# Kernel optimization log

Hardware: AMD Instinct MI355X
Metric: run time of the kernel (lower is better)

The kernel has to match this reference:

```python
import jax, jax.numpy as jnp
import numpy as np
import math

N_COARSE, N_FINE = 8192, 32768
DEC_DIM, ENC_DIM, OUT_DIM, K = 256, 128, 128, 16
LN_EPS = 1e-5


def setup_inputs() -> dict:
    key = jax.random.key(0)
    ks = jax.random.split(key, 16)
    s = lambda fan_in: 1.0 / math.sqrt(fan_in)
    return {
        "decoder_features": jax.random.normal(ks[0], (N_COARSE, DEC_DIM), jnp.float32),
        "decoder_pos": jax.random.normal(ks[1], (N_COARSE, 3), jnp.float32),
        "encoder_features": jax.random.normal(ks[2], (N_FINE, ENC_DIM), jnp.float32),
        "encoder_pos": jax.random.normal(ks[3], (N_FINE, 3), jnp.float32),
        "encoder_labels": jax.random.randint(ks[4], (N_FINE,), 0, 13, jnp.int64),
        # params (torch nn.Linear default init scale)
        "Wq": jax.random.uniform(ks[5], (DEC_DIM, ENC_DIM), jnp.float32, -s(ENC_DIM), s(ENC_DIM)),
        "bq": jnp.zeros((DEC_DIM,), jnp.float32),
        "Wk": jax.random.uniform(ks[6], (DEC_DIM, DEC_DIM), jnp.float32, -s(DEC_DIM), s(DEC_DIM)),
        "bk": jnp.zeros((DEC_DIM,), jnp.float32),
        "Wv": jax.random.uniform(ks[7], (DEC_DIM, DEC_DIM), jnp.float32, -s(DEC_DIM), s(DEC_DIM)),
        "bv": jnp.zeros((DEC_DIM,), jnp.float32),
        "W1": jax.random.uniform(ks[8], (OUT_DIM, DEC_DIM + ENC_DIM), jnp.float32, -s(DEC_DIM + ENC_DIM), s(DEC_DIM + ENC_DIM)),
        "b1": jnp.zeros((OUT_DIM,), jnp.float32),
        "W2": jax.random.uniform(ks[9], (OUT_DIM, OUT_DIM), jnp.float32, -s(OUT_DIM), s(OUT_DIM)),
        "b2": jnp.zeros((OUT_DIM,), jnp.float32),
        "ln_g": jnp.ones((OUT_DIM,), jnp.float32),
        "ln_b": jnp.zeros((OUT_DIM,), jnp.float32),
    }


def _knn_indices(encoder_pos, decoder_pos, k):
    # For each fine (encoder) point, k nearest coarse (decoder) points.
    # squared distances [N_fine, N_coarse]
    d2 = (
        jnp.sum(encoder_pos * encoder_pos, axis=1, keepdims=True)
        - 2.0 * encoder_pos @ decoder_pos.T
        + jnp.sum(decoder_pos * decoder_pos, axis=1)[None, :]
    )
    _, idx = jax.lax.top_k(-d2, k)  # [N_fine, K]
    return idx


def reference(decoder_features, decoder_pos, encoder_features, encoder_pos,
              encoder_labels, Wq, bq, Wk, bk, Wv, bv, W1, b1, W2, b2, ln_g, ln_b):
    idx = _knn_indices(encoder_pos, decoder_pos, K)            # [Nf, K]
    nbr = decoder_features[idx]                                 # [Nf, K, Dd]
    query = encoder_features @ Wq.T + bq                        # [Nf, Dd]
    keys = nbr @ Wk.T + bk                                      # [Nf, K, Dd]
    values = nbr @ Wv.T + bv                                    # [Nf, K, Dd]
    scores = jnp.einsum('nd,nkd->nk', query, keys) / math.sqrt(DEC_DIM)
    # segment softmax over edges grouped by fine target == softmax over K
    weights = jax.nn.softmax(scores, axis=-1)                   # [Nf, K]
    agg = jnp.einsum('nk,nkd->nd', weights, values)             # [Nf, Dd]
    combined = jnp.concatenate([agg, encoder_features], axis=-1)
    h = jax.nn.relu(combined @ W1.T + b1)
    up = h @ W2.T + b2                                          # [Nf, out]
    mu = jnp.mean(up, axis=-1, keepdims=True)
    var = jnp.var(up, axis=-1, keepdims=True)
    out = (up - mu) * jax.lax.rsqrt(var + LN_EPS) * ln_g + ln_b
    # dropout is identity in eval mode
    return (out, encoder_pos, encoder_labels)
```

## Files before the change

kernel.cpp:

```cpp
#include <hip/hip_runtime.h>
#include <hip/hip_bf16.h>

typedef __hip_bfloat16 bf16;
typedef unsigned short u16;

#define NC 8192
#define NF 32768
#define KNN 16
#define FMAXV 3.402823466e+38f

__device__ __forceinline__ float bfbits2f(u16 u){
  union { unsigned u; float f; } x; x.u = ((unsigned)u) << 16; return x.f;
}

__global__ __launch_bounds__(256) void k_prep(const float* __restrict__ dpos,
                                              const float* __restrict__ W1,
                                              const float* __restrict__ W2,
                                              float4* __restrict__ pos4,
                                              float4* __restrict__ W1eSa,
                                              float4* __restrict__ W1eSb,
                                              float4* __restrict__ W2Sa,
                                              float4* __restrict__ W2Sb){
  int g = blockIdx.x * 256 + threadIdx.x;
  if (g < 8192){
    float x = dpos[g * 3 + 0], y = dpos[g * 3 + 1], z = dpos[g * 3 + 2];
    float dd = __fadd_rn(__fadd_rn(__fmul_rn(x,x), __fmul_rn(y,y)), __fmul_rn(z,z));
    pos4[g] = make_float4(x, y, z, dd * 0.5f);
  } else if (g < 10240){
    int f = g - 8192; int c4 = f >> 6, jg = f & 63;
    W1eSa[f] = ((const float4*)(W1 + (size_t)(2 * jg) * 384 + 256))[c4];
  } else if (g < 12288){
    int f = g - 10240; int c4 = f >> 6, jg = f & 63;
    W1eSb[f] = ((const float4*)(W1 + (size_t)(2 * jg + 1) * 384 + 256))[c4];
  } else if (g < 14336){
    int f = g - 12288; int c4 = f >> 6, jg = f & 63;
    W2Sa[f] = ((const float4*)(W2 + (size_t)(2 * jg) * 128))[c4];
  } else if (g < 16384){
    int f = g - 14336; int c4 = f >> 6, jg = f & 63;
    W2Sb[f] = ((const float4*)(W2 + (size_t)(2 * jg + 1) * 128))[c4];
  }
}

__global__ __launch_bounds__(256) void k_wprod(const float* __restrict__ Wk,
                                               const float* __restrict__ Wv,
                                               const float* __restrict__ Wq,
                                               const float* __restrict__ W1,
                                               const float* __restrict__ bk,
                                               const float* __restrict__ bv,
                                               const float* __restrict__ bq,
                                               float* __restrict__ WkqS,
                                               float* __restrict__ WvuS,
                                               float* __restrict__ bkq,
                                               float* __restrict__ bvu,
                                               float* __restrict__ wbq,
                                               float* __restrict__ sbq){
  __shared__ float red[256];
  int b = blockIdx.x, t = threadIdx.x;
  if (b < 128){
    int c = b;
    float acc = 0.f;
    for (int j = 0; j < 256; ++j)
      acc = fmaf(Wk[(size_t)j * 256 + t], Wq[(size_t)j * 128 + c], acc);
    WkqS[(size_t)((t >> 2) * 128 + c) * 4 + (t & 3)] = acc;
    red[t] = bk[t] * Wq[(size_t)t * 128 + c];
    __syncthreads();
    for (int s = 128; s > 0; s >>= 1){ if (t < s) red[t] += red[t + s]; __syncthreads(); }
    if (t == 0) bkq[c] = red[0];
  } else if (b < 256){
    int h = b - 128;
    float acc = 0.f;
    for (int c2 = 0; c2 < 256; ++c2)
      acc = fmaf(Wv[(size_t)c2 * 256 + t], W1[(size_t)h * 384 + c2], acc);
    WvuS[(size_t)((t >> 2) * 128 + h) * 4 + (t & 3)] = acc;
    red[t] = bv[t] * W1[(size_t)h * 384 + t];
    __syncthreads();
    for (int s = 128; s > 0; s >>= 1){ if (t < s) red[t] += red[t + s]; __syncthreads(); }
    if (t == 0) bvu[h] = red[0];
  } else {
    float acc = 0.f;
    for (int j = 0; j < 256; ++j)
      acc = fmaf(Wk[(size_t)j * 256 + t], bq[j], acc);
    wbq[t] = acc;
    red[t] = bk[t] * bq[t];
    __syncthreads();
    for (int s = 128; s > 0; s >>= 1){ if (t < s) red[t] += red[t + s]; __syncthreads(); }
    if (t == 0) sbq[0] = red[0];
  }
}

__global__ __launch_bounds__(256) void k_dec(const float* __restrict__ df,
                                             const float4* __restrict__ WkqS,
                                             const float4* __restrict__ WvuS,
                                             const float* __restrict__ bkq,
                                             const float* __restrict__ bvu,
                                             const float* __restrict__ wbq,
                                             const float* __restrict__ sbq,
                                             bf16* __restrict__ Zd, bf16* __restrict__ Ud,
                                             float* __restrict__ bqK){
  __shared__ float part[16][16];
  int t = threadIdx.x;
  int g0 = blockIdx.x * 16;
  int half = __builtin_amdgcn_readfirstlane(t >> 7);
  int c = t & 127;
  const float4* W = half ? WvuS : WkqS;
  float acc[16];
  #pragma unroll
  for (int p = 0; p < 16; ++p) acc[p] = 0.f;
  for (int j4 = 0; j4 < 64; ++j4){
    float4 w = W[j4 * 128 + c];
    #pragma unroll
    for (int p = 0; p < 16; ++p){
      float4 a = ((const float4*)(df + (size_t)(g0 + p) * 256))[j4];
      acc[p] += w.x*a.x + w.y*a.y + w.z*a.z + w.w*a.w;
    }
  }
  float bias = half ? bvu[c] : bkq[c];
  bf16* dst = half ? Ud : Zd;
  #pragma unroll
  for (int p = 0; p < 16; ++p)
    dst[(size_t)(g0 + p) * 128 + c] = __float2bfloat16(acc[p] + bias);
  {
    int r = t >> 4, seg = t & 15;
    float s = 0.f;
    const float* dr = df + (size_t)(g0 + r) * 256 + seg * 16;
    const float* wq = wbq + seg * 16;
    #pragma unroll
    for (int e = 0; e < 16; ++e) s = fmaf(dr[e], wq[e], s);
    part[r][seg] = s;
  }
  __syncthreads();
  if (t < 16){
    float s = sbq[0];
    #pragma unroll
    for (int seg = 0; seg < 16; ++seg) s += part[t][seg];
    bqK[g0 + t] = s;
  }
}

__global__ __launch_bounds__(256) void k_attn(const float* __restrict__ epos,
                                              const float4* __restrict__ pos4,
                                              const float* __restrict__ ef,
                                              const bf16* __restrict__ Zd,
                                              const bf16* __restrict__ Ud,
                                              const float* __restrict__ bqK,
                                              bf16* __restrict__ hagg){
  __shared__ float smin[8 * 64];
  __shared__ float tauLDS[8];
  __shared__ int   cnt[8];
  __shared__ float lval[8][64];
  __shared__ int   lidx[8][64];

  int t = threadIdx.x, lane = t & 63, w = t >> 6;
  int n0 = blockIdx.x * 8;
  float nex[8], ney[8], nez[8];
  #pragma unroll
  for (int p = 0; p < 8; ++p){
    nex[p] = -epos[(n0 + p) * 3 + 0];
    ney[p] = -epos[(n0 + p) * 3 + 1];
    nez[p] = -epos[(n0 + p) * 3 + 2];
  }
  const float4* base = pos4 + w * 2048;

  float vmin[8] = {FMAXV,FMAXV,FMAXV,FMAXV,FMAXV,FMAXV,FMAXV,FMAXV};
  #pragma unroll 2
  for (int s = 0; s < 32; ++s){
    float4 P = base[s * 64 + lane];
    #pragma unroll
    for (int p = 0; p < 8; ++p){
      float val = fmaf(nez[p], P.z, fmaf(ney[p], P.y, fmaf(nex[p], P.x, P.w)));
      vmin[p] = fminf(vmin[p], val);
    }
  }
  #pragma unroll
  for (int k = 2; k <= 64; k <<= 1){
    #pragma unroll
    for (int j = k >> 1; j > 0; j >>= 1){
      bool keepmin = ((lane & j) == 0) == ((lane & k) == 0);
      #pragma unroll
      for (int p = 0; p < 8; ++p){
        float pv = __shfl_xor(vmin[p], j);
        vmin[p] = keepmin ? fminf(vmin[p], pv) : fmaxf(vmin[p], pv);
      }
    }
  }
  if (lane < 16){
    #pragma unroll
    for (int p = 0; p < 8; ++p) smin[p * 64 + w * 16 + lane] = vmin[p];
  }
  if (t < 8) cnt[t] = 0;
  __syncthreads();
  #pragma unroll
  for (int u = 0; u < 2; ++u){
    int p = w * 2 + u;
    float v = smin[p * 64 + lane];
    #pragma unroll
    for (int k = 2; k <= 64; k <<= 1){
      #pragma unroll
      for (int j = k >> 1; j > 0; j >>= 1){
        float pv = __shfl_xor(v, j);
        bool keepmin = ((lane & j) == 0) == ((lane & k) == 0);
        v = keepmin ? fminf(v, pv) : fmaxf(v, pv);
      }
    }
    if (lane == 16) tauLDS[p] = v;
  }
  __syncthreads();
  float tau0[8];
  #pragma unroll
  for (int p = 0; p < 8; ++p) tau0[p] = tauLDS[p];

  #pragma unroll 2
  for (int s = 0; s < 32; ++s){
    float4 P = base[s * 64 + lane];
    int cand = w * 2048 + s * 64 + lane;
    #pragma unroll
    for (int p = 0; p < 8; ++p){
      float val = fmaf(nez[p], P.z, fmaf(ney[p], P.y, fmaf(nex[p], P.x, P.w)));
      if (val <= tau0[p]){
        int slot = atomicAdd(&cnt[p], 1);
        if (slot < 64){ lval[p][slot] = val; lidx[p][slot] = cand; }
      }
    }
  }
  __syncthreads();

  for (int u = 0; u < 2; ++u){
    int p = w * 2 + u;
    int n = n0 + p;
    int c = cnt[p]; if (c > 64) c = 64;
    float v  = (lane < c) ? lval[p][lane] : FMAXV;
    int   id = (lane < c) ? lidx[p][lane] : 0x7fffffff;
    #pragma unroll
    for (int k = 2; k <= 64; k <<= 1){
      #pragma unroll
      for (int j = k >> 1; j > 0; j >>= 1){
        float pv  = __shfl_xor(v, j);
        int   pid = __shfl_xor(id, j);
        bool keepmin = ((lane & j) == 0) == ((lane & k) == 0);
        bool pless = (pv < v) || (pv == v && pid < id);
        bool take = keepmin ? pless : !pless;
        if (take){ v = pv; id = pid; }
      }
    }
    int topi = id;

    float2 eu = *(const float2*)(ef + (size_t)n * 128 + lane * 2);
    float sc = -FMAXV;
    #pragma unroll
    for (int k = 0; k < KNN; ++k){
      int ik = __shfl(topi, k);
      ushort2 zu = *(const ushort2*)((const u16*)Zd + (size_t)ik * 128 + lane * 2);
      float pr = eu.x * bfbits2f(zu.x) + eu.y * bfbits2f(zu.y);
      #pragma unroll
      for (int off = 32; off >= 1; off >>= 1) pr += __shfl_xor(pr, off);
      float bz = bqK[ik];
      if (lane == k) sc = (pr + bz) * (1.0f / 16.0f);
    }
    float mx = sc;
    #pragma unroll
    for (int off = 8; off >= 1; off >>= 1) mx = fmaxf(mx, __shfl_xor(mx, off));
    float e = (lane < KNN) ? __expf(sc - mx) : 0.f;
    float l = e;
    #pragma unroll
    for (int off = 8; off >= 1; off >>= 1) l += __shfl_xor(l, off);
    float wgt = (lane < KNN) ? (e / l) : 0.f;

    float a0 = 0.f, a1 = 0.f;
    #pragma unroll
    for (int k = 0; k < KNN; ++k){
      int ik = __shfl(topi, k);
      float wk = __shfl(wgt, k);
      ushort2 uu = *(const ushort2*)((const u16*)Ud + (size_t)ik * 128 + lane * 2);
      a0 = fmaf(wk, bfbits2f(uu.x), a0);
      a1 = fmaf(wk, bfbits2f(uu.y), a1);
    }
    bf16* hr = hagg + (size_t)n * 128 + lane * 2;
    hr[0] = __float2bfloat16(a0);
    hr[1] = __float2bfloat16(a1);
  }
}

__global__ __launch_bounds__(256) void k_mlp(const bf16* __restrict__ hagg,
                                             const float* __restrict__ ef,
                                             const float4* __restrict__ W1eSa,
                                             const float4* __restrict__ W1eSb,
                                             const float* __restrict__ b1,
                                             const float4* __restrict__ W2Sa,
                                             const float4* __restrict__ W2Sb,
                                             const float* __restrict__ b2,
                                             const float* __restrict__ lng, const float* __restrict__ lnb,
                                             const float* __restrict__ epos, const int* __restrict__ lab,
                                             float* __restrict__ out){
  __shared__ float hbuf[16 * 128];
  __shared__ float ubuf[16 * 128];
  __shared__ float stats[32];
  int t = threadIdx.x;
  int n0 = blockIdx.x * 16;
  {
    int gid = blockIdx.x * 256 + t;
    if (gid < NF){
      float* op = out + (size_t)NF * 128;
      op[gid * 3 + 0] = epos[gid * 3 + 0];
      op[gid * 3 + 1] = epos[gid * 3 + 1];
      op[gid * 3 + 2] = epos[gid * 3 + 2];
      out[(size_t)NF * 128 + (size_t)NF * 3 + gid] = (float)lab[gid];
    }
  }
  int jg = t & 63;
  int pg4 = __builtin_amdgcn_readfirstlane((t >> 6) * 4);
  int j0 = jg * 2;
  float acc[2][4];
  #pragma unroll
  for (int a = 0; a < 2; ++a)
    #pragma unroll
    for (int p = 0; p < 4; ++p) acc[a][p] = 0.f;
  for (int c4 = 0; c4 < 32; ++c4){
    float4 wa = W1eSa[c4 * 64 + jg];
    float4 wb = W1eSb[c4 * 64 + jg];
    #pragma unroll
    for (int p = 0; p < 4; ++p){
      float4 x = ((const float4*)(ef + (size_t)(n0 + pg4 + p) * 128))[c4];
      acc[0][p] += wa.x*x.x + wa.y*x.y + wa.z*x.z + wa.w*x.w;
      acc[1][p] += wb.x*x.x + wb.y*x.y + wb.z*x.z + wb.w*x.w;
    }
  }
  float b1a = b1[j0], b1b = b1[j0 + 1];
  #pragma unroll
  for (int p = 0; p < 4; ++p){
    size_t row = (size_t)(n0 + pg4 + p);
    ushort2 hgv = *(const ushort2*)((const u16*)hagg + row * 128 + j0);
    hbuf[(pg4 + p) * 128 + j0]     = fmaxf(acc[0][p] + b1a + bfbits2f(hgv.x), 0.f);
    hbuf[(pg4 + p) * 128 + j0 + 1] = fmaxf(acc[1][p] + b1b + bfbits2f(hgv.y), 0.f);
  }
  __syncthreads();
  float acc2[2][4];
  #pragma unroll
  for (int a = 0; a < 2; ++a)
    #pragma unroll
    for (int p = 0; p < 4; ++p) acc2[a][p] = 0.f;
  const float4* hb4 = (const float4*)hbuf;
  for (int c4 = 0; c4 < 32; ++c4){
    float4 wa = W2Sa[c4 * 64 + jg];
    float4 wb = W2Sb[c4 * 64 + jg];
    #pragma unroll
    for (int p = 0; p < 4; ++p){
      float4 x = hb4[(pg4 + p) * 32 + c4];
      acc2[0][p] += wa.x*x.x + wa.y*x.y + wa.z*x.z + wa.w*x.w;
      acc2[1][p] += wb.x*x.x + wb.y*x.y + wb.z*x.z + wb.w*x.w;
    }
  }
  float b2a = b2[j0], b2b = b2[j0 + 1];
  float u[2][4];
  #pragma unroll
  for (int p = 0; p < 4; ++p){
    u[0][p] = acc2[0][p] + b2a;
    u[1][p] = acc2[1][p] + b2b;
    ubuf[(pg4 + p) * 128 + j0]     = u[0][p];
    ubuf[(pg4 + p) * 128 + j0 + 1] = u[1][p];
  }
  __syncthreads();
  {
    int p = t >> 4, qi = t & 15;
    const float* ub = &ubuf[p * 128 + qi * 8];
    float s = 0.f, s2 = 0.f;
    #pragma unroll
    for (int e2i = 0; e2i < 8; ++e2i){ float v = ub[e2i]; s += v; s2 += v * v; }
    #pragma unroll
    for (int off = 1; off < 16; off <<= 1){ s += __shfl_xor(s, off); s2 += __shfl_xor(s2, off); }
    if (qi == 0){
      float mu = s * (1.f / 128.f);
      float var = s2 * (1.f / 128.f) - mu * mu;
      stats[p] = mu;
      stats[16 + p] = rsqrtf(fmaxf(var, 0.f) + 1e-5f);
    }
  }
  __syncthreads();
  float ga = lng[j0], gb = lng[j0 + 1];
  float ba = lnb[j0], bbv = lnb[j0 + 1];
  #pragma unroll
  for (int p = 0; p < 4; ++p){
    float mu = stats[pg4 + p], rs = stats[16 + pg4 + p];
    out[(size_t)(n0 + pg4 + p) * 128 + j0]     = (u[0][p] - mu) * rs * ga + ba;
    out[(size_t)(n0 + pg4 + p) * 128 + j0 + 1] = (u[1][p] - mu) * rs * gb + bbv;
  }
}

extern "C" void kernel_launch(void* const* d_in, const int* in_sizes, int n_in,
                              void* d_out, int out_size, void* d_ws, size_t ws_size,
                              hipStream_t stream){
  const float* df   = (const float*)d_in[0];
  const float* dpos = (const float*)d_in[1];
  const float* ef   = (const float*)d_in[2];
  const float* epos = (const float*)d_in[3];
  const int*   lab  = (const int*)d_in[4];
  const float* Wq = (const float*)d_in[5];
  const float* bq = (const float*)d_in[6];
  const float* Wk = (const float*)d_in[7];
  const float* bk = (const float*)d_in[8];
  const float* Wv = (const float*)d_in[9];
  const float* bv = (const float*)d_in[10];
  const float* W1 = (const float*)d_in[11];
  const float* b1 = (const float*)d_in[12];
  const float* W2 = (const float*)d_in[13];
  const float* b2 = (const float*)d_in[14];
  const float* lng = (const float*)d_in[15];
  const float* lnb = (const float*)d_in[16];
  float* out = (float*)d_out;

  char* wsb = (char*)d_ws;
  float4* pos4  = (float4*)(wsb);
  bf16*   Zd    = (bf16*)(wsb + 131072);
  bf16*   Ud    = (bf16*)(wsb + 2228224);
  float*  bqK   = (float*)(wsb + 4325376);
  bf16*   hagg  = (bf16*)(wsb + 4358144);
  float4* W1eSa = (float4*)(wsb + 12746752);
  float4* W1eSb = (float4*)(wsb + 12779520);
  float4* W2Sa  = (float4*)(wsb + 12812288);
  float4* W2Sb  = (float4*)(wsb + 12845056);
  float*  WkqS  = (float*)(wsb + 12877824);
  float*  WvuS  = (float*)(wsb + 13008896);
  float*  bkq   = (float*)(wsb + 13139968);
  float*  bvu   = (float*)(wsb + 13140480);
  float*  wbq   = (float*)(wsb + 13140992);
  float*  sbq   = (float*)(wsb + 13142016);

  k_prep  <<<64,  256, 0, stream>>>(dpos, W1, W2, pos4, W1eSa, W1eSb, W2Sa, W2Sb);
  k_wprod <<<257, 256, 0, stream>>>(Wk, Wv, Wq, W1, bk, bv, bq, WkqS, WvuS, bkq, bvu, wbq, sbq);
  k_dec   <<<NC / 16, 256, 0, stream>>>(df, (const float4*)WkqS, (const float4*)WvuS, bkq, bvu, wbq, sbq, Zd, Ud, bqK);
  k_attn  <<<NF / 8, 256, 0, stream>>>(epos, pos4, ef, Zd, Ud, bqK, hagg);
  k_mlp   <<<NF / 16, 256, 0, stream>>>(hagg, ef, W1eSa, W1eSb, b1, W2Sa, W2Sb, b2, lng, lnb, epos, lab, out);
  (void)in_sizes; (void)n_in; (void)out_size; (void)ws_size;
}
```

Measured before the change: 360.9 us.

## Pack decoder positions in pairs for packed FMA and restructure score computation

Decoder positions are stored as interleaved pairs (x0,x1,y0,y1 / z0,z1,w0,w1), so the kNN distance scans can use v_pk_fma_f32 and handle two candidates per instruction. The query-key score loop is rewritten so each lane handles one neighbour slice with 16-byte Zd loads and only two shuffle reductions, replacing sixteen full-wave reductions. The encoder feature row is staged in LDS for this, and the hagg store is vectorised. The risk is extra register pressure from the paired accumulators, plus LDS reuse of smin that depends on the manual waitcnt.

```diff
diff --git a/kernel.cpp b/kernel.cpp
--- a/kernel.cpp
+++ b/kernel.cpp
@@ -3,6 +3,7 @@
 
 typedef __hip_bfloat16 bf16;
 typedef unsigned short u16;
+typedef float f32x2 __attribute__((ext_vector_type(2)));
 
 #define NC 8192
 #define NF 32768
@@ -12,30 +13,43 @@
 __device__ __forceinline__ float bfbits2f(u16 u){
   union { unsigned u; float f; } x; x.u = ((unsigned)u) << 16; return x.f;
 }
+__device__ __forceinline__ float asfloat(unsigned u){
+  union { unsigned u; float f; } x; x.u = u; return x.f;
+}
+__device__ __forceinline__ f32x2 pk_fma(f32x2 a, f32x2 b, f32x2 c){
+  f32x2 d;
+  asm("v_pk_fma_f32 %0, %1, %2, %3" : "=v"(d) : "v"(a), "v"(b), "v"(c));
+  return d;
+}
 
 __global__ __launch_bounds__(256) void k_prep(const float* __restrict__ dpos,
                                               const float* __restrict__ W1,
                                               const float* __restrict__ W2,
-                                              float4* __restrict__ pos4,
+                                              float4* __restrict__ posP,
                                               float4* __restrict__ W1eSa,
                                               float4* __restrict__ W1eSb,
                                               float4* __restrict__ W2Sa,
                                               float4* __restrict__ W2Sb){
   int g = blockIdx.x * 256 + threadIdx.x;
-  if (g < 8192){
-    float x = dpos[g * 3 + 0], y = dpos[g * 3 + 1], z = dpos[g * 3 + 2];
-    float dd = __fadd_rn(__fadd_rn(__fmul_rn(x,x), __fmul_rn(y,y)), __fmul_rn(z,z));
-    pos4[g] = make_float4(x, y, z, dd * 0.5f);
-  } else if (g < 10240){
+  if (g < 4096){
+    const float2* dp2 = (const float2*)(dpos + (size_t)g * 6);
+    float2 a = dp2[0], b = dp2[1], c = dp2[2];
+    float x0 = a.x, y0 = a.y, z0 = b.x;
+    float x1 = b.y, y1 = c.x, z1 = c.y;
+    float dd0 = __fadd_rn(__fadd_rn(__fmul_rn(x0,x0), __fmul_rn(y0,y0)), __fmul_rn(z0,z0));
+    float dd1 = __fadd_rn(__fadd_rn(__fmul_rn(x1,x1), __fmul_rn(y1,y1)), __fmul_rn(z1,z1));
+    posP[g * 2]     = make_float4(x0, x1, y0, y1);
+    posP[g * 2 + 1] = make_float4(z0, z1, dd0 * 0.5f, dd1 * 0.5f);
+  } else if (g >= 8192 && g < 10240){
     int f = g - 8192; int c4 = f >> 6, jg = f & 63;
     W1eSa[f] = ((const float4*)(W1 + (size_t)(2 * jg) * 384 + 256))[c4];
-  } else if (g < 12288){
+  } else if (g >= 10240 && g < 12288){
     int f = g - 10240; int c4 = f >> 6, jg = f & 63;
     W1eSb[f] = ((const float4*)(W1 + (size_t)(2 * jg + 1) * 384 + 256))[c4];
-  } else if (g < 14336){
+  } else if (g >= 12288 && g < 14336){
     int f = g - 12288; int c4 = f >> 6, jg = f & 63;
     W2Sa[f] = ((const float4*)(W2 + (size_t)(2 * jg) * 128))[c4];
-  } else if (g < 16384){
+  } else if (g >= 14336){
     int f = g - 14336; int c4 = f >> 6, jg = f & 63;
     W2Sb[f] = ((const float4*)(W2 + (size_t)(2 * jg + 1) * 128))[c4];
   }
@@ -138,7 +152,7 @@
 }
 
 __global__ __launch_bounds__(256) void k_attn(const float* __restrict__ epos,
-                                              const float4* __restrict__ pos4,
+                                              const float4* __restrict__ posP,
                                               const float* __restrict__ ef,
                                               const bf16* __restrict__ Zd,
                                               const bf16* __restrict__ Ud,
@@ -152,25 +166,39 @@
 
   int t = threadIdx.x, lane = t & 63, w = t >> 6;
   int n0 = blockIdx.x * 8;
-  float nex[8], ney[8], nez[8];
+  f32x2 nex2[8], ney2[8], nez2[8];
   #pragma unroll
   for (int p = 0; p < 8; ++p){
-    nex[p] = -epos[(n0 + p) * 3 + 0];
-    ney[p] = -epos[(n0 + p) * 3 + 1];
-    nez[p] = -epos[(n0 + p) * 3 + 2];
-  }
-  const float4* base = pos4 + w * 2048;
-
-  float vmin[8] = {FMAXV,FMAXV,FMAXV,FMAXV,FMAXV,FMAXV,FMAXV,FMAXV};
+    float nx = -epos[(n0 + p) * 3 + 0];
+    float ny = -epos[(n0 + p) * 3 + 1];
+    float nz = -epos[(n0 + p) * 3 + 2];
+    nex2[p].x = nx; nex2[p].y = nx;
+    ney2[p].x = ny; ney2[p].y = ny;
+    nez2[p].x = nz; nez2[p].y = nz;
+  }
+  const float4* base = posP + w * 2048;
+
+  f32x2 vmin2[8];
+  #pragma unroll
+  for (int p = 0; p < 8; ++p){ vmin2[p].x = FMAXV; vmin2[p].y = FMAXV; }
   #pragma unroll 2
-  for (int s = 0; s < 32; ++s){
-    float4 P = base[s * 64 + lane];
+  for (int s = 0; s < 16; ++s){
+    int q2 = (s * 64 + lane) * 2;
+    float4 XY = base[q2], ZW = base[q2 + 1];
+    f32x2 X = {XY.x, XY.y}, Y = {XY.z, XY.w}, Z = {ZW.x, ZW.y}, W = {ZW.z, ZW.w};
     #pragma unroll
     for (int p = 0; p < 8; ++p){
-      float val = fmaf(nez[p], P.z, fmaf(ney[p], P.y, fmaf(nex[p], P.x, P.w)));
-      vmin[p] = fminf(vmin[p], val);
-    }
-  }
+      f32x2 v2 = pk_fma(nex2[p], X, W);
+      v2 = pk_fma(ney2[p], Y, v2);
+      v2 = pk_fma(nez2[p], Z, v2);
+      vmin2[p].x = fminf(vmin2[p].x, v2.x);
+      vmin2[p].y = fminf(vmin2[p].y, v2.y);
+    }
+  }
+  float vmin[8];
+  #pragma unroll
+  for (int p = 0; p < 8; ++p) vmin[p] = fminf(vmin2[p].x, vmin2[p].y);
+
   #pragma unroll
   for (int k = 2; k <= 64; k <<= 1){
     #pragma unroll
@@ -210,15 +238,23 @@
   for (int p = 0; p < 8; ++p) tau0[p] = tauLDS[p];
 
   #pragma unroll 2
-  for (int s = 0; s < 32; ++s){
-    float4 P = base[s * 64 + lane];
-    int cand = w * 2048 + s * 64 + lane;
+  for (int s = 0; s < 16; ++s){
+    int q = s * 64 + lane;
+    float4 XY = base[q * 2], ZW = base[q * 2 + 1];
+    f32x2 X = {XY.x, XY.y}, Y = {XY.z, XY.w}, Z = {ZW.x, ZW.y}, W = {ZW.z, ZW.w};
+    int cand0 = w * 2048 + q * 2;
     #pragma unroll
     for (int p = 0; p < 8; ++p){
-      float val = fmaf(nez[p], P.z, fmaf(ney[p], P.y, fmaf(nex[p], P.x, P.w)));
-      if (val <= tau0[p]){
+      f32x2 v2 = pk_fma(nex2[p], X, W);
+      v2 = pk_fma(ney2[p], Y, v2);
+      v2 = pk_fma(nez2[p], Z, v2);
+      if (v2.x <= tau0[p]){
         int slot = atomicAdd(&cnt[p], 1);
-        if (slot < 64){ lval[p][slot] = val; lidx[p][slot] = cand; }
+        if (slot < 64){ lval[p][slot] = v2.x; lidx[p][slot] = cand0; }
+      }
+      if (v2.y <= tau0[p]){
+        int slot = atomicAdd(&cnt[p], 1);
+        if (slot < 64){ lval[p][slot] = v2.y; lidx[p][slot] = cand0 + 1; }
       }
     }
   }
@@ -244,18 +280,27 @@
     }
     int topi = id;
 
-    float2 eu = *(const float2*)(ef + (size_t)n * 128 + lane * 2);
-    float sc = -FMAXV;
-    #pragma unroll
-    for (int k = 0; k < KNN; ++k){
-      int ik = __shfl(topi, k);
-      ushort2 zu = *(const ushort2*)((const u16*)Zd + (size_t)ik * 128 + lane * 2);
-      float pr = eu.x * bfbits2f(zu.x) + eu.y * bfbits2f(zu.y);
-      #pragma unroll
-      for (int off = 32; off >= 1; off >>= 1) pr += __shfl_xor(pr, off);
-      float bz = bqK[ik];
-      if (lane == k) sc = (pr + bz) * (1.0f / 16.0f);
-    }
+    *(float2*)&smin[w * 128 + lane * 2] = *(const float2*)(ef + (size_t)n * 128 + lane * 2);
+    asm volatile("s_waitcnt lgkmcnt(0)" ::: "memory");
+
+    int kk = lane & 15, part = lane >> 4;
+    int ik = __shfl(topi, kk);
+    const uint4*  zr = (const uint4*)((const u16*)Zd + (size_t)ik * 128) + part * 4;
+    const float4* e4 = (const float4*)(smin + w * 128) + part * 8;
+    float pr = 0.f;
+    #pragma unroll
+    for (int i = 0; i < 4; ++i){
+      uint4 z = zr[i];
+      float4 ea = e4[2 * i], eb = e4[2 * i + 1];
+      pr = fmaf(ea.x, asfloat(z.x << 16), pr); pr = fmaf(ea.y, asfloat(z.x & 0xffff0000u), pr);
+      pr = fmaf(ea.z, asfloat(z.y << 16), pr); pr = fmaf(ea.w, asfloat(z.y & 0xffff0000u), pr);
+      pr = fmaf(eb.x, asfloat(z.z << 16), pr); pr = fmaf(eb.y, asfloat(z.z & 0xffff0000u), pr);
+      pr = fmaf(eb.z, asfloat(z.w << 16), pr); pr = fmaf(eb.w, asfloat(z.w & 0xffff0000u), pr);
+    }
+    pr += __shfl_xor(pr, 16);
+    pr += __shfl_xor(pr, 32);
+    float sc = (pr + bqK[ik]) * (1.0f / 16.0f);
+
     float mx = sc;
     #pragma unroll
     for (int off = 8; off >= 1; off >>= 1) mx = fmaxf(mx, __shfl_xor(mx, off));
@@ -268,15 +313,15 @@
     float a0 = 0.f, a1 = 0.f;
     #pragma unroll
     for (int k = 0; k < KNN; ++k){
-      int ik = __shfl(topi, k);
+      int ikk = __shfl(topi, k);
       float wk = __shfl(wgt, k);
-      ushort2 uu = *(const ushort2*)((const u16*)Ud + (size_t)ik * 128 + lane * 2);
+      ushort2 uu = *(const ushort2*)((const u16*)Ud + (size_t)ikk * 128 + lane * 2);
       a0 = fmaf(wk, bfbits2f(uu.x), a0);
       a1 = fmaf(wk, bfbits2f(uu.y), a1);
     }
-    bf16* hr = hagg + (size_t)n * 128 + lane * 2;
-    hr[0] = __float2bfloat16(a0);
-    hr[1] = __float2bfloat16(a1);
+    bf16 h0 = __float2bfloat16(a0), h1 = __float2bfloat16(a1);
+    ushort2 st; st.x = *(u16*)&h0; st.y = *(u16*)&h1;
+    *(ushort2*)(hagg + (size_t)n * 128 + lane * 2) = st;
   }
 }
 
@@ -408,7 +453,7 @@
   float* out = (float*)d_out;
 
   char* wsb = (char*)d_ws;
-  float4* pos4  = (float4*)(wsb);
+  float4* posP  = (float4*)(wsb);
   bf16*   Zd    = (bf16*)(wsb + 131072);
   bf16*   Ud    = (bf16*)(wsb + 2228224);
   float*  bqK   = (float*)(wsb + 4325376);
@@ -424,10 +469,10 @@
   float*  wbq   = (float*)(wsb + 13140992);
   float*  sbq   = (float*)(wsb + 13142016);
 
-  k_prep  <<<64,  256, 0, stream>>>(dpos, W1, W2, pos4, W1eSa, W1eSb, W2Sa, W2Sb);
+  k_prep  <<<64,  256, 0, stream>>>(dpos, W1, W2, posP, W1eSa, W1eSb, W2Sa, W2Sb);
   k_wprod <<<257, 256, 0, stream>>>(Wk, Wv, Wq, W1, bk, bv, bq, WkqS, WvuS, bkq, bvu, wbq, sbq);
   k_dec   <<<NC / 16, 256, 0, stream>>>(df, (const float4*)WkqS, (const float4*)WvuS, bkq, bvu, wbq, sbq, Zd, Ud, bqK);
-  k_attn  <<<NF / 8, 256, 0, stream>>>(epos, pos4, ef, Zd, Ud, bqK, hagg);
+  k_attn  <<<NF / 8, 256, 0, stream>>>(epos, posP, ef, Zd, Ud, bqK, hagg);
   k_mlp   <<<NF / 16, 256, 0, stream>>>(hagg, ef, W1eSa, W1eSb, b1, W2Sa, W2Sb, b2, lng, lnb, epos, lab, out);
   (void)in_sizes; (void)n_in; (void)out_size; (void)ws_size;
 }
```

After: 335.2 us. 1.08x faster.
